# Performance work log

Hardware: AMD Instinct MI355X
Metric: run time of the kernel (lower is better)

## Reference

```python
import jax, jax.numpy as jnp
import numpy as np

N_NODES = 100000


def _sage_conv(x, src, dst, W_l, b_l, W_r, num_nodes):
    # PyG SAGEConv (aggr='mean'): out = lin_l(mean_j x_j) + lin_r(x)
    msg = x[src]                                                   # [E, d] gather
    s = jax.ops.segment_sum(msg, dst, num_segments=num_nodes)      # [N, d]
    cnt = jax.ops.segment_sum(jnp.ones((src.shape[0], 1), x.dtype), dst,
                              num_segments=num_nodes)              # [N, 1]
    agg = s / jnp.maximum(cnt, 1)                                  # mean, 0 if no neighbors
    return agg @ W_l.T + b_l + x @ W_r.T


def setup_inputs() -> dict:
    key = jax.random.key(0)
    ks = jax.random.split(key, 8)
    d = 64
    E = 1600000
    scale = 1.0 / np.sqrt(d)
    x = jax.random.normal(ks[0], (N_NODES, d), dtype=jnp.float32)
    edge_index = jax.random.randint(ks[1], (2, E), 0, N_NODES, dtype=jnp.int64)
    W1_l = jax.random.normal(ks[2], (d, d), dtype=jnp.float32) * scale
    b1_l = jnp.zeros((d,), dtype=jnp.float32)
    W1_r = jax.random.normal(ks[3], (d, d), dtype=jnp.float32) * scale
    W2_l = jax.random.normal(ks[4], (d, d), dtype=jnp.float32) * scale
    b2_l = jnp.zeros((d,), dtype=jnp.float32)
    W2_r = jax.random.normal(ks[5], (d, d), dtype=jnp.float32) * scale
    return {"x": x, "edge_index": edge_index, "W1_l": W1_l, "b1_l": b1_l,
            "W1_r": W1_r, "W2_l": W2_l, "b2_l": b2_l, "W2_r": W2_r}


def reference(x, edge_index, W1_l, b1_l, W1_r, W2_l, b2_l, W2_r):
    src, dst = edge_index[0], edge_index[1]
    h = jax.nn.relu(_sage_conv(x, src, dst, W1_l, b1_l, W1_r, N_NODES))
    h = jax.nn.relu(_sage_conv(h, src, dst, W2_l, b2_l, W2_r, N_NODES))
    return h
```

## Files before the change

kernel.cpp:

```cpp
#include <hip/hip_runtime.h>
#include <hip/hip_fp16.h>


#define NFEAT 64
#define NPB 128
#define NBUCK 782
#define MAXPB 2560
#define TILE 4096

typedef _Float16 h8 __attribute__((ext_vector_type(8)));
typedef _Float16 h4 __attribute__((ext_vector_type(4)));
typedef float f4 __attribute__((ext_vector_type(4)));
typedef float f2 __attribute__((ext_vector_type(2)));

__device__ inline h8 cvt8f(const float* p) {
  float4 lo = *(const float4*)p;
  float4 hi = *(const float4*)(p + 4);
  h8 f;
  f[0]=(_Float16)lo.x; f[1]=(_Float16)lo.y; f[2]=(_Float16)lo.z; f[3]=(_Float16)lo.w;
  f[4]=(_Float16)hi.x; f[5]=(_Float16)hi.y; f[6]=(_Float16)hi.z; f[7]=(_Float16)hi.w;
  return f;
}

__device__ inline void acc16(float* a, uint4 r) {
  f2 t;
  t = __builtin_amdgcn_cvt_pk_f32_fp8((int)r.x, false); a[0]+=t[0];  a[1]+=t[1];
  t = __builtin_amdgcn_cvt_pk_f32_fp8((int)r.x, true);  a[2]+=t[0];  a[3]+=t[1];
  t = __builtin_amdgcn_cvt_pk_f32_fp8((int)r.y, false); a[4]+=t[0];  a[5]+=t[1];
  t = __builtin_amdgcn_cvt_pk_f32_fp8((int)r.y, true);  a[6]+=t[0];  a[7]+=t[1];
  t = __builtin_amdgcn_cvt_pk_f32_fp8((int)r.z, false); a[8]+=t[0];  a[9]+=t[1];
  t = __builtin_amdgcn_cvt_pk_f32_fp8((int)r.z, true);  a[10]+=t[0]; a[11]+=t[1];
  t = __builtin_amdgcn_cvt_pk_f32_fp8((int)r.w, false); a[12]+=t[0]; a[13]+=t[1];
  t = __builtin_amdgcn_cvt_pk_f32_fp8((int)r.w, true);  a[14]+=t[0]; a[15]+=t[1];
}

__device__ inline void gather_team(float* a, const int* __restrict__ csr,
                                   const unsigned char* __restrict__ Z,
                                   int start, int deg, int q, int team) {
  int nfull = deg >> 2;
  for (int k = team; k < nfull; k += 2) {
    int j = start + k * 4;
    int n0 = csr[j + 0];
    int n1 = csr[j + 1];
    int n2 = csr[j + 2];
    int n3 = csr[j + 3];
    uint4 r0 = *(const uint4*)(Z + (size_t)n0 * NFEAT + q * 16);
    uint4 r1 = *(const uint4*)(Z + (size_t)n1 * NFEAT + q * 16);
    uint4 r2 = *(const uint4*)(Z + (size_t)n2 * NFEAT + q * 16);
    uint4 r3 = *(const uint4*)(Z + (size_t)n3 * NFEAT + q * 16);
    acc16(a, r0); acc16(a, r1); acc16(a, r2); acc16(a, r3);
  }
  int rem = deg & 3;
  if (rem && ((nfull & 1) == team)) {
    int j = start + nfull * 4;
    for (int i = 0; i < rem; ++i) {
      int nb = csr[j + i];
      uint4 r = *(const uint4*)(Z + (size_t)nb * NFEAT + q * 16);
      acc16(a, r);
    }
  }
}

__global__ __launch_bounds__(512) void build_gemm1_k(
    const int* __restrict__ src, const int* __restrict__ dst,
    int* __restrict__ gcur, int* __restrict__ pairs, int E, int sb,
    const float* __restrict__ X, const float* __restrict__ Wl,
    const float* __restrict__ Wr, const float* __restrict__ bias,
    unsigned char* __restrict__ Zf8, __half* __restrict__ Ph, int n) {
  int tid = threadIdx.x;
  if ((int)blockIdx.x < sb) {
    __shared__ int lcnt[NBUCK];
    __shared__ int loff[NBUCK];
    __shared__ int lcur[NBUCK];
    __shared__ int lbase[NBUCK];
    __shared__ int s_packed[TILE];
    __shared__ unsigned short s_b[TILE];

    int tileStart = blockIdx.x * TILE;
    int tileCnt = E - tileStart; if (tileCnt > TILE) tileCnt = TILE;

    for (int t = tid; t < NBUCK; t += 512) lcnt[t] = 0;
    __syncthreads();

    int ep[8], eb[8];
    int base = tileStart + tid * 8;
    int ne = 0;
    if (base + 7 < E) {
      int4 a0 = *(const int4*)(src + base);
      int4 a1 = *(const int4*)(src + base + 4);
      int4 b0 = *(const int4*)(dst + base);
      int4 b1 = *(const int4*)(dst + base + 4);
      int es[8] = {a0.x,a0.y,a0.z,a0.w,a1.x,a1.y,a1.z,a1.w};
      int ed[8] = {b0.x,b0.y,b0.z,b0.w,b1.x,b1.y,b1.z,b1.w};
#pragma unroll
      for (int j = 0; j < 8; ++j) {
        eb[j] = ed[j] >> 7;
        ep[j] = es[j] | ((ed[j] & 127) << 17);
      }
      ne = 8;
    } else {
      for (int j = 0; j < 8 && base + j < E; ++j) {
        int s = src[base + j], d = dst[base + j];
        eb[j] = d >> 7;
        ep[j] = s | ((d & 127) << 17);
        ++ne;
      }
    }
    for (int j = 0; j < ne; ++j) atomicAdd(&lcnt[eb[j]], 1);
    __syncthreads();

    if (tid < 64) {
      int carry = 0;
      for (int cb = 0; cb < NBUCK; cb += 64) {
        int i = cb + tid;
        int v = (i < NBUCK) ? lcnt[i] : 0;
        int x = v;
#pragma unroll
        for (int d = 1; d < 64; d <<= 1) {
          int y = __shfl_up(x, d);
          if (tid >= d) x += y;
        }
        if (i < NBUCK) { int e = x - v + carry; loff[i] = e; lcur[i] = e; }
        carry += __shfl(x, 63);
      }
    }
    __syncthreads();

    for (int t = tid; t < NBUCK; t += 512) {
      int v = lcnt[t];
      if (v) lbase[t] = atomicAdd(&gcur[t], v);
    }
    __syncthreads();

    for (int j = 0; j < ne; ++j) {
      int b = eb[j];
      int slot = atomicAdd(&lcur[b], 1);
      s_packed[slot] = ep[j];
      s_b[slot] = (unsigned short)b;
    }
    __syncthreads();

    for (int k = tid; k < tileCnt; k += 512) {
      int b = s_b[k];
      int g = lbase[b] + (k - loff[b]);
      if (g < MAXPB) pairs[(size_t)b * MAXPB + g] = s_packed[k];
    }
  } else {
    int wave = tid >> 6, lane = tid & 63;
    int m = lane & 15, quad = lane >> 4;
    int row0 = (((int)blockIdx.x - sb) * 8 + wave) * 16;
    if (row0 >= n) return;

    h8 wf[2][4][2];
#pragma unroll
    for (int mat = 0; mat < 2; ++mat) {
      const float* W = mat ? Wr : Wl;
#pragma unroll
      for (int t = 0; t < 4; ++t)
#pragma unroll
        for (int s = 0; s < 2; ++s)
          wf[mat][t][s] = cvt8f(W + (t * 16 + m) * 64 + s * 32 + quad * 8);
    }

    int rowm = row0 + m; if (rowm > n - 1) rowm = n - 1;
    const float* xp = X + (size_t)rowm * 64 + quad * 8;
    h8 af0 = cvt8f(xp);
    h8 af1 = cvt8f(xp + 32);

    f4 accz[4], accp[4];
#pragma unroll
    for (int t = 0; t < 4; ++t) {
      f4 z; z[0]=0.f; z[1]=0.f; z[2]=0.f; z[3]=0.f;
      float4 bl = *(const float4*)(bias + t * 16 + quad * 4);
      f4 p; p[0]=bl.x; p[1]=bl.y; p[2]=bl.z; p[3]=bl.w;
      z = __builtin_amdgcn_mfma_f32_16x16x32_f16(wf[0][t][0], af0, z, 0, 0, 0);
      z = __builtin_amdgcn_mfma_f32_16x16x32_f16(wf[0][t][1], af1, z, 0, 0, 0);
      p = __builtin_amdgcn_mfma_f32_16x16x32_f16(wf[1][t][0], af0, p, 0, 0, 0);
      p = __builtin_amdgcn_mfma_f32_16x16x32_f16(wf[1][t][1], af1, p, 0, 0, 0);
      accz[t] = z;
      accp[t] = p;
    }

    if (row0 + m < n) {
      size_t node = (size_t)(row0 + m);
#pragma unroll
      for (int t = 0; t < 4; ++t) {
        h4 pv;
#pragma unroll
        for (int r = 0; r < 4; ++r) pv[r] = (_Float16)accp[t][r];
        *(h4*)(Ph + node * NFEAT + t * 16 + quad * 4) = pv;
        int v = 0;
        v = __builtin_amdgcn_cvt_pk_fp8_f32(accz[t][0], accz[t][1], v, false);
        v = __builtin_amdgcn_cvt_pk_fp8_f32(accz[t][2], accz[t][3], v, true);
        *(int*)(Zf8 + node * NFEAT + t * 16 + quad * 4) = v;
      }
    }
  }
}

__global__ __launch_bounds__(512) void regroup_k(const int* __restrict__ gcur,
                                                 const int* __restrict__ pairs,
                                                 int* __restrict__ csr,
                                                 int* __restrict__ off,
                                                 int* __restrict__ cnt,
                                                 float* __restrict__ inv, int n) {
  __shared__ int lcnt[NPB];
  __shared__ int lofs[NPB];
  __shared__ int lcur[NPB];
  __shared__ int stage[MAXPB];

  int tid = threadIdx.x;
  int b = blockIdx.x;
  int nbase = b << 7;
  int nn = n - nbase; if (nn > NPB) nn = NPB;
  if (nn <= 0) return;

  int m = gcur[b]; if (m > MAXPB) m = MAXPB;
  const int* seg = pairs + (size_t)b * MAXPB;

  if (tid < NPB) lcnt[tid] = 0;
  __syncthreads();

  for (int e = tid; e < m; e += 512)
    atomicAdd(&lcnt[(seg[e] >> 17) & 127], 1);
  __syncthreads();

  if (tid < 64) {
    int carry = 0;
#pragma unroll
    for (int cb = 0; cb < NPB; cb += 64) {
      int i = cb + tid;
      int v = lcnt[i];
      int x = v;
#pragma unroll
      for (int d = 1; d < 64; d <<= 1) {
        int y = __shfl_up(x, d);
        if (tid >= d) x += y;
      }
      int e = x - v + carry;
      lofs[i] = e; lcur[i] = e;
      carry += __shfl(x, 63);
    }
  }
  __syncthreads();

  for (int e = tid; e < m; e += 512) {
    int p = seg[e];
    int slot = atomicAdd(&lcur[(p >> 17) & 127], 1);
    stage[slot] = p & 0x1FFFF;
  }
  __syncthreads();

  for (int k = tid; k < m; k += 512) csr[(size_t)b * MAXPB + k] = stage[k];
  for (int t = tid; t < nn; t += 512) {
    int c = lcnt[t];
    cnt[nbase + t] = c;
    off[nbase + t] = b * MAXPB + lofs[t];
    inv[nbase + t] = 1.0f / (float)(c > 1 ? c : 1);
  }
}

__global__ __launch_bounds__(256) void aggemm_k(
    const int* __restrict__ off, const int* __restrict__ cnt,
    const float* __restrict__ inv, const int* __restrict__ csr,
    const unsigned char* __restrict__ Z, const __half* __restrict__ Pin,
    const float* __restrict__ Wl, const float* __restrict__ Wr,
    const float* __restrict__ bias,
    unsigned char* __restrict__ Zout, __half* __restrict__ Pout, int n) {
  __shared__ _Float16 Hs[32][72];
  int tid = threadIdx.x;
  int nbase = blockIdx.x * 32;
  int nl   = tid >> 3;
  int t8   = tid & 7;
  int q    = t8 & 3;
  int team = t8 >> 2;
  int node = nbase + nl;

  float a[16];
#pragma unroll
  for (int i = 0; i < 16; ++i) a[i] = 0.f;

  if (node < n) {
    gather_team(a, csr, Z, off[node], cnt[node], q, team);
  }
#pragma unroll
  for (int i = 0; i < 16; ++i) a[i] += __shfl_xor(a[i], 4);

  if (node < n) {
    float iv = inv[node];
    if (team == 0) {
      h8 p0 = *(const h8*)(Pin + (size_t)node * NFEAT + q * 16);
      h8 h0;
#pragma unroll
      for (int i = 0; i < 8; ++i)
        h0[i] = (_Float16)fmaxf(fmaf(a[i], iv, (float)p0[i]), 0.f);
      *(h8*)&Hs[nl][q * 16] = h0;
    } else {
      h8 p1 = *(const h8*)(Pin + (size_t)node * NFEAT + q * 16 + 8);
      h8 h1;
#pragma unroll
      for (int i = 0; i < 8; ++i)
        h1[i] = (_Float16)fmaxf(fmaf(a[8 + i], iv, (float)p1[i]), 0.f);
      *(h8*)&Hs[nl][q * 16 + 8] = h1;
    }
  } else if (team == 0) {
    h8 zz;
#pragma unroll
    for (int i = 0; i < 8; ++i) zz[i] = (_Float16)0.f;
    *(h8*)&Hs[nl][q * 16] = zz;
    *(h8*)&Hs[nl][q * 16 + 8] = zz;
  }
  __syncthreads();

  int wave = tid >> 6, lane = tid & 63;
  if (wave >= 2) return;
  int m = lane & 15, quad = lane >> 4;
  int row0 = wave * 16;

  h8 wf[2][4][2];
#pragma unroll
  for (int mat = 0; mat < 2; ++mat) {
    const float* W = mat ? Wr : Wl;
#pragma unroll
    for (int t = 0; t < 4; ++t)
#pragma unroll
      for (int s = 0; s < 2; ++s)
        wf[mat][t][s] = cvt8f(W + (t * 16 + m) * 64 + s * 32 + quad * 8);
  }

  h8 af0 = *(const h8*)&Hs[row0 + m][quad * 8];
  h8 af1 = *(const h8*)&Hs[row0 + m][32 + quad * 8];

  f4 accz[4], accp[4];
#pragma unroll
  for (int t = 0; t < 4; ++t) {
    f4 z; z[0]=0.f; z[1]=0.f; z[2]=0.f; z[3]=0.f;
    float4 bl = *(const float4*)(bias + t * 16 + quad * 4);
    f4 p; p[0]=bl.x; p[1]=bl.y; p[2]=bl.z; p[3]=bl.w;
    z = __builtin_amdgcn_mfma_f32_16x16x32_f16(wf[0][t][0], af0, z, 0, 0, 0);
    z = __builtin_amdgcn_mfma_f32_16x16x32_f16(wf[0][t][1], af1, z, 0, 0, 0);
    p = __builtin_amdgcn_mfma_f32_16x16x32_f16(wf[1][t][0], af0, p, 0, 0, 0);
    p = __builtin_amdgcn_mfma_f32_16x16x32_f16(wf[1][t][1], af1, p, 0, 0, 0);
    accz[t] = z;
    accp[t] = p;
  }

  int gnode = nbase + row0 + m;
  if (gnode < n) {
    size_t nodeix = (size_t)gnode;
#pragma unroll
    for (int t = 0; t < 4; ++t) {
      h4 pv;
#pragma unroll
      for (int r = 0; r < 4; ++r) pv[r] = (_Float16)accp[t][r];
      *(h4*)(Pout + nodeix * NFEAT + t * 16 + quad * 4) = pv;
      int v = 0;
      v = __builtin_amdgcn_cvt_pk_fp8_f32(accz[t][0], accz[t][1], v, false);
      v = __builtin_amdgcn_cvt_pk_fp8_f32(accz[t][2], accz[t][3], v, true);
      *(int*)(Zout + nodeix * NFEAT + t * 16 + quad * 4) = v;
    }
  }
}

__global__ __launch_bounds__(256) void agg2_k(const int* __restrict__ off,
                                              const int* __restrict__ cnt,
                                              const float* __restrict__ inv,
                                              const int* __restrict__ csr,
                                              const unsigned char* __restrict__ Z,
                                              const __half* __restrict__ Pin,
                                              float* __restrict__ out, int n) {
  int t = blockIdx.x * 256 + threadIdx.x;
  int node = t >> 3;
  if (node >= n) return;
  int t8   = t & 7;
  int q    = t8 & 3;
  int team = t8 >> 2;

  float a[16];
#pragma unroll
  for (int i = 0; i < 16; ++i) a[i] = 0.f;

  gather_team(a, csr, Z, off[node], cnt[node], q, team);
#pragma unroll
  for (int i = 0; i < 16; ++i) a[i] += __shfl_xor(a[i], 4);

  float iv = inv[node];
  float* op = out + (size_t)node * NFEAT + q * 16;
  if (team == 0) {
    h8 p0 = *(const h8*)(Pin + (size_t)node * NFEAT + q * 16);
    float4 r0, r1;
    r0.x = fmaxf(fmaf(a[0], iv, (float)p0[0]), 0.f);
    r0.y = fmaxf(fmaf(a[1], iv, (float)p0[1]), 0.f);
    r0.z = fmaxf(fmaf(a[2], iv, (float)p0[2]), 0.f);
    r0.w = fmaxf(fmaf(a[3], iv, (float)p0[3]), 0.f);
    r1.x = fmaxf(fmaf(a[4], iv, (float)p0[4]), 0.f);
    r1.y = fmaxf(fmaf(a[5], iv, (float)p0[5]), 0.f);
    r1.z = fmaxf(fmaf(a[6], iv, (float)p0[6]), 0.f);
    r1.w = fmaxf(fmaf(a[7], iv, (float)p0[7]), 0.f);
    *(float4*)(op + 0) = r0;
    *(float4*)(op + 4) = r1;
  } else {
    h8 p1 = *(const h8*)(Pin + (size_t)node * NFEAT + q * 16 + 8);
    float4 r2, r3;
    r2.x = fmaxf(fmaf(a[8],  iv, (float)p1[0]), 0.f);
    r2.y = fmaxf(fmaf(a[9],  iv, (float)p1[1]), 0.f);
    r2.z = fmaxf(fmaf(a[10], iv, (float)p1[2]), 0.f);
    r2.w = fmaxf(fmaf(a[11], iv, (float)p1[3]), 0.f);
    r3.x = fmaxf(fmaf(a[12], iv, (float)p1[4]), 0.f);
    r3.y = fmaxf(fmaf(a[13], iv, (float)p1[5]), 0.f);
    r3.z = fmaxf(fmaf(a[14], iv, (float)p1[6]), 0.f);
    r3.w = fmaxf(fmaf(a[15], iv, (float)p1[7]), 0.f);
    *(float4*)(op + 8)  = r2;
    *(float4*)(op + 12) = r3;
  }
}

extern "C" void kernel_launch(void* const* d_in, const int* in_sizes, int n_in,
                              void* d_out, int out_size, void* d_ws, size_t ws_size,
                              hipStream_t stream) {
  const float* x   = (const float*)d_in[0];
  const int*   ei  = (const int*)d_in[1];
  const float* W1l = (const float*)d_in[2];
  const float* b1  = (const float*)d_in[3];
  const float* W1r = (const float*)d_in[4];
  const float* W2l = (const float*)d_in[5];
  const float* b2  = (const float*)d_in[6];
  const float* W2r = (const float*)d_in[7];
  float* out = (float*)d_out;

  int N = in_sizes[0] / NFEAT;
  int E = in_sizes[1] / 2;
  const int* srcp = ei;
  const int* dstp = ei + E;

  char* w = (char*)d_ws;
  int*           pairs = (int*)w;           w += (size_t)NBUCK * MAXPB * 4;
  int*           csr   = (int*)w;           w += (size_t)NBUCK * MAXPB * 4;
  unsigned char* Z1    = (unsigned char*)w; w += (size_t)N * NFEAT;
  __half*        P1    = (__half*)w;        w += (size_t)N * NFEAT * 2;
  unsigned char* Z2    = (unsigned char*)w; w += (size_t)N * NFEAT;
  __half*        P2    = (__half*)w;        w += (size_t)N * NFEAT * 2;
  int*           off   = (int*)w;           w += (size_t)N * 4;
  int*           cnt   = (int*)w;           w += (size_t)N * 4;
  float*         inv   = (float*)w;         w += (size_t)N * 4;
  int*           gcur  = (int*)w;           w += NBUCK * 4;
  if ((size_t)(w - (char*)d_ws) > ws_size) return;

  hipMemsetAsync(gcur, 0, NBUCK * 4, stream);

  int sb  = (E + TILE - 1) / TILE;
  int gb1 = (N + 127) / 128;

  build_gemm1_k<<<sb + gb1, 512, 0, stream>>>(srcp, dstp, gcur, pairs, E, sb,
                                              x, W1l, W1r, b1, Z1, P1, N);
  regroup_k<<<NBUCK, 512, 0, stream>>>(gcur, pairs, csr, off, cnt, inv, N);
  aggemm_k<<<(N + 31) / 32, 256, 0, stream>>>(off, cnt, inv, csr, Z1, P1,
                                              W2l, W2r, b2, Z2, P2, N);
  agg2_k<<<(N * 8 + 255) / 256, 256, 0, stream>>>(off, cnt, inv, csr, Z2, P2,
                                                  out, N);
}
```

Measured before the change: 232.9 us.

## Fuse CSR regroup with layer-2 aggregation GEMM and split layer-2 features into planes

Merges the regroup kernel and the first aggregation+GEMM kernel into one 1024-thread block per 128-node bucket, reading neighbor indices straight from shared memory instead of writing and re-reading the CSR from global memory. This also removes a kernel launch. Layer-2 fp8 features are now stored as two 32-byte half planes, and the final aggregation kernel runs one block set per plane with four teams per node, so each plane's gather footprint is smaller and more cache-friendly. The cost is larger blocks with lower occupancy and bucket-granularity parallelism (782 blocks) for the gather phase.

```diff
diff --git a/kernel.cpp b/kernel.cpp
--- a/kernel.cpp
+++ b/kernel.cpp
@@ -32,33 +32,6 @@
   t = __builtin_amdgcn_cvt_pk_f32_fp8((int)r.z, true);  a[10]+=t[0]; a[11]+=t[1];
   t = __builtin_amdgcn_cvt_pk_f32_fp8((int)r.w, false); a[12]+=t[0]; a[13]+=t[1];
   t = __builtin_amdgcn_cvt_pk_f32_fp8((int)r.w, true);  a[14]+=t[0]; a[15]+=t[1];
-}
-
-__device__ inline void gather_team(float* a, const int* __restrict__ csr,
-                                   const unsigned char* __restrict__ Z,
-                                   int start, int deg, int q, int team) {
-  int nfull = deg >> 2;
-  for (int k = team; k < nfull; k += 2) {
-    int j = start + k * 4;
-    int n0 = csr[j + 0];
-    int n1 = csr[j + 1];
-    int n2 = csr[j + 2];
-    int n3 = csr[j + 3];
-    uint4 r0 = *(const uint4*)(Z + (size_t)n0 * NFEAT + q * 16);
-    uint4 r1 = *(const uint4*)(Z + (size_t)n1 * NFEAT + q * 16);
-    uint4 r2 = *(const uint4*)(Z + (size_t)n2 * NFEAT + q * 16);
-    uint4 r3 = *(const uint4*)(Z + (size_t)n3 * NFEAT + q * 16);
-    acc16(a, r0); acc16(a, r1); acc16(a, r2); acc16(a, r3);
-  }
-  int rem = deg & 3;
-  if (rem && ((nfull & 1) == team)) {
-    int j = start + nfull * 4;
-    for (int i = 0; i < rem; ++i) {
-      int nb = csr[j + i];
-      uint4 r = *(const uint4*)(Z + (size_t)nb * NFEAT + q * 16);
-      acc16(a, r);
-    }
-  }
 }
 
 __global__ __launch_bounds__(512) void build_gemm1_k(
@@ -198,16 +171,20 @@
   }
 }
 
-__global__ __launch_bounds__(512) void regroup_k(const int* __restrict__ gcur,
-                                                 const int* __restrict__ pairs,
-                                                 int* __restrict__ csr,
-                                                 int* __restrict__ off,
-                                                 int* __restrict__ cnt,
-                                                 float* __restrict__ inv, int n) {
+__global__ __launch_bounds__(1024) void raggemm_k(
+    const int* __restrict__ gcur, const int* __restrict__ pairs,
+    int* __restrict__ csr, int* __restrict__ off,
+    int* __restrict__ cnt, float* __restrict__ inv,
+    const unsigned char* __restrict__ Z, const __half* __restrict__ Pin,
+    const float* __restrict__ Wl, const float* __restrict__ Wr,
+    const float* __restrict__ bias,
+    unsigned char* __restrict__ Zlo, unsigned char* __restrict__ Zhi,
+    __half* __restrict__ Pout, int n) {
   __shared__ int lcnt[NPB];
   __shared__ int lofs[NPB];
   __shared__ int lcur[NPB];
   __shared__ int stage[MAXPB];
+  __shared__ _Float16 Hs[NPB][72];
 
   int tid = threadIdx.x;
   int b = blockIdx.x;
@@ -221,7 +198,7 @@
   if (tid < NPB) lcnt[tid] = 0;
   __syncthreads();
 
-  for (int e = tid; e < m; e += 512)
+  for (int e = tid; e < m; e += 1024)
     atomicAdd(&lcnt[(seg[e] >> 17) & 127], 1);
   __syncthreads();
 
@@ -244,32 +221,21 @@
   }
   __syncthreads();
 
-  for (int e = tid; e < m; e += 512) {
+  for (int e = tid; e < m; e += 1024) {
     int p = seg[e];
     int slot = atomicAdd(&lcur[(p >> 17) & 127], 1);
     stage[slot] = p & 0x1FFFF;
   }
   __syncthreads();
 
-  for (int k = tid; k < m; k += 512) csr[(size_t)b * MAXPB + k] = stage[k];
-  for (int t = tid; t < nn; t += 512) {
+  for (int k = tid; k < m; k += 1024) csr[(size_t)b * MAXPB + k] = stage[k];
+  for (int t = tid; t < nn; t += 1024) {
     int c = lcnt[t];
     cnt[nbase + t] = c;
     off[nbase + t] = b * MAXPB + lofs[t];
     inv[nbase + t] = 1.0f / (float)(c > 1 ? c : 1);
   }
-}
-
-__global__ __launch_bounds__(256) void aggemm_k(
-    const int* __restrict__ off, const int* __restrict__ cnt,
-    const float* __restrict__ inv, const int* __restrict__ csr,
-    const unsigned char* __restrict__ Z, const __half* __restrict__ Pin,
-    const float* __restrict__ Wl, const float* __restrict__ Wr,
-    const float* __restrict__ bias,
-    unsigned char* __restrict__ Zout, __half* __restrict__ Pout, int n) {
-  __shared__ _Float16 Hs[32][72];
-  int tid = threadIdx.x;
-  int nbase = blockIdx.x * 32;
+
   int nl   = tid >> 3;
   int t8   = tid & 7;
   int q    = t8 & 3;
@@ -280,14 +246,37 @@
 #pragma unroll
   for (int i = 0; i < 16; ++i) a[i] = 0.f;
 
+  int deg = 0, start = 0;
+  if (node < n) { deg = lcnt[nl]; start = lofs[nl]; }
+  {
+    int nfull = deg >> 2;
+    for (int k = team; k < nfull; k += 2) {
+      int j = start + k * 4;
+      int n0 = stage[j + 0];
+      int n1 = stage[j + 1];
+      int n2 = stage[j + 2];
+      int n3 = stage[j + 3];
+      uint4 r0 = *(const uint4*)(Z + (size_t)n0 * NFEAT + q * 16);
+      uint4 r1 = *(const uint4*)(Z + (size_t)n1 * NFEAT + q * 16);
+      uint4 r2 = *(const uint4*)(Z + (size_t)n2 * NFEAT + q * 16);
+      uint4 r3 = *(const uint4*)(Z + (size_t)n3 * NFEAT + q * 16);
+      acc16(a, r0); acc16(a, r1); acc16(a, r2); acc16(a, r3);
+    }
+    int rem = deg & 3;
+    if (rem && ((nfull & 1) == team)) {
+      int j = start + nfull * 4;
+      for (int i = 0; i < rem; ++i) {
+        int nb = stage[j + i];
+        uint4 r = *(const uint4*)(Z + (size_t)nb * NFEAT + q * 16);
+        acc16(a, r);
+      }
+    }
+  }
+#pragma unroll
+  for (int i = 0; i < 16; ++i) a[i] += __shfl_xor(a[i], 4);
+
   if (node < n) {
-    gather_team(a, csr, Z, off[node], cnt[node], q, team);
-  }
-#pragma unroll
-  for (int i = 0; i < 16; ++i) a[i] += __shfl_xor(a[i], 4);
-
-  if (node < n) {
-    float iv = inv[node];
+    float iv = 1.0f / (float)(deg > 1 ? deg : 1);
     if (team == 0) {
       h8 p0 = *(const h8*)(Pin + (size_t)node * NFEAT + q * 16);
       h8 h0;
@@ -313,8 +302,8 @@
   __syncthreads();
 
   int wave = tid >> 6, lane = tid & 63;
-  if (wave >= 2) return;
-  int m = lane & 15, quad = lane >> 4;
+  if (wave >= 8) return;
+  int mm = lane & 15, quad = lane >> 4;
   int row0 = wave * 16;
 
   h8 wf[2][4][2];
@@ -325,11 +314,11 @@
     for (int t = 0; t < 4; ++t)
 #pragma unroll
       for (int s = 0; s < 2; ++s)
-        wf[mat][t][s] = cvt8f(W + (t * 16 + m) * 64 + s * 32 + quad * 8);
-  }
-
-  h8 af0 = *(const h8*)&Hs[row0 + m][quad * 8];
-  h8 af1 = *(const h8*)&Hs[row0 + m][32 + quad * 8];
+        wf[mat][t][s] = cvt8f(W + (t * 16 + mm) * 64 + s * 32 + quad * 8);
+  }
+
+  h8 af0 = *(const h8*)&Hs[row0 + mm][quad * 8];
+  h8 af1 = *(const h8*)&Hs[row0 + mm][32 + quad * 8];
 
   f4 accz[4], accp[4];
 #pragma unroll
@@ -345,7 +334,7 @@
     accp[t] = p;
   }
 
-  int gnode = nbase + row0 + m;
+  int gnode = nbase + row0 + mm;
   if (gnode < n) {
     size_t nodeix = (size_t)gnode;
 #pragma unroll
@@ -357,7 +346,8 @@
       int v = 0;
       v = __builtin_amdgcn_cvt_pk_fp8_f32(accz[t][0], accz[t][1], v, false);
       v = __builtin_amdgcn_cvt_pk_fp8_f32(accz[t][2], accz[t][3], v, true);
-      *(int*)(Zout + nodeix * NFEAT + t * 16 + quad * 4) = v;
+      unsigned char* zp = (t < 2) ? Zlo : Zhi;
+      *(int*)(zp + nodeix * 32 + (t & 1) * 16 + quad * 4) = v;
     }
   }
 }
@@ -366,42 +356,70 @@
                                               const int* __restrict__ cnt,
                                               const float* __restrict__ inv,
                                               const int* __restrict__ csr,
-                                              const unsigned char* __restrict__ Z,
+                                              const unsigned char* __restrict__ Zlo,
+                                              const unsigned char* __restrict__ Zhi,
                                               const __half* __restrict__ Pin,
-                                              float* __restrict__ out, int n) {
-  int t = blockIdx.x * 256 + threadIdx.x;
-  int node = t >> 3;
+                                              float* __restrict__ out,
+                                              int n, int nchunk) {
+  int bi = blockIdx.x;
+  int plane = (bi >= nchunk) ? 1 : 0;
+  int chunk = plane ? bi - nchunk : bi;
+  int tid = threadIdx.x;
+  int nl = tid >> 3;
+  int node = chunk * 32 + nl;
   if (node >= n) return;
-  int t8   = t & 7;
-  int q    = t8 & 3;
-  int team = t8 >> 2;
+  int t8   = tid & 7;
+  int half = t8 & 1;
+  int team = t8 >> 1;
+  const unsigned char* Zp = plane ? Zhi : Zlo;
 
   float a[16];
 #pragma unroll
   for (int i = 0; i < 16; ++i) a[i] = 0.f;
 
-  gather_team(a, csr, Z, off[node], cnt[node], q, team);
+  int start = off[node];
+  int deg = cnt[node];
+  int nfull = deg >> 2;
+  for (int k = team; k < nfull; k += 4) {
+    int j = start + k * 4;
+    int n0 = csr[j + 0];
+    int n1 = csr[j + 1];
+    int n2 = csr[j + 2];
+    int n3 = csr[j + 3];
+    uint4 r0 = *(const uint4*)(Zp + (size_t)n0 * 32 + half * 16);
+    uint4 r1 = *(const uint4*)(Zp + (size_t)n1 * 32 + half * 16);
+    uint4 r2 = *(const uint4*)(Zp + (size_t)n2 * 32 + half * 16);
+    uint4 r3 = *(const uint4*)(Zp + (size_t)n3 * 32 + half * 16);
+    acc16(a, r0); acc16(a, r1); acc16(a, r2); acc16(a, r3);
+  }
+  int rem = deg & 3;
+  if (rem && ((nfull & 3) == team)) {
+    int j = start + nfull * 4;
+    for (int i = 0; i < rem; ++i) {
+      int nb = csr[j + i];
+      uint4 r = *(const uint4*)(Zp + (size_t)nb * 32 + half * 16);
+      acc16(a, r);
+    }
+  }
+#pragma unroll
+  for (int i = 0; i < 16; ++i) a[i] += __shfl_xor(a[i], 2);
 #pragma unroll
   for (int i = 0; i < 16; ++i) a[i] += __shfl_xor(a[i], 4);
 
-  float iv = inv[node];
-  float* op = out + (size_t)node * NFEAT + q * 16;
   if (team == 0) {
-    h8 p0 = *(const h8*)(Pin + (size_t)node * NFEAT + q * 16);
-    float4 r0, r1;
-    r0.x = fmaxf(fmaf(a[0], iv, (float)p0[0]), 0.f);
-    r0.y = fmaxf(fmaf(a[1], iv, (float)p0[1]), 0.f);
-    r0.z = fmaxf(fmaf(a[2], iv, (float)p0[2]), 0.f);
-    r0.w = fmaxf(fmaf(a[3], iv, (float)p0[3]), 0.f);
-    r1.x = fmaxf(fmaf(a[4], iv, (float)p0[4]), 0.f);
-    r1.y = fmaxf(fmaf(a[5], iv, (float)p0[5]), 0.f);
-    r1.z = fmaxf(fmaf(a[6], iv, (float)p0[6]), 0.f);
-    r1.w = fmaxf(fmaf(a[7], iv, (float)p0[7]), 0.f);
-    *(float4*)(op + 0) = r0;
-    *(float4*)(op + 4) = r1;
-  } else {
-    h8 p1 = *(const h8*)(Pin + (size_t)node * NFEAT + q * 16 + 8);
-    float4 r2, r3;
+    float iv = inv[node];
+    int fbase = plane * 32 + half * 16;
+    h8 p0 = *(const h8*)(Pin + (size_t)node * NFEAT + fbase);
+    h8 p1 = *(const h8*)(Pin + (size_t)node * NFEAT + fbase + 8);
+    float4 r0, r1, r2, r3;
+    r0.x = fmaxf(fmaf(a[0],  iv, (float)p0[0]), 0.f);
+    r0.y = fmaxf(fmaf(a[1],  iv, (float)p0[1]), 0.f);
+    r0.z = fmaxf(fmaf(a[2],  iv, (float)p0[2]), 0.f);
+    r0.w = fmaxf(fmaf(a[3],  iv, (float)p0[3]), 0.f);
+    r1.x = fmaxf(fmaf(a[4],  iv, (float)p0[4]), 0.f);
+    r1.y = fmaxf(fmaf(a[5],  iv, (float)p0[5]), 0.f);
+    r1.z = fmaxf(fmaf(a[6],  iv, (float)p0[6]), 0.f);
+    r1.w = fmaxf(fmaf(a[7],  iv, (float)p0[7]), 0.f);
     r2.x = fmaxf(fmaf(a[8],  iv, (float)p1[0]), 0.f);
     r2.y = fmaxf(fmaf(a[9],  iv, (float)p1[1]), 0.f);
     r2.z = fmaxf(fmaf(a[10], iv, (float)p1[2]), 0.f);
@@ -410,6 +428,9 @@
     r3.y = fmaxf(fmaf(a[13], iv, (float)p1[5]), 0.f);
     r3.z = fmaxf(fmaf(a[14], iv, (float)p1[6]), 0.f);
     r3.w = fmaxf(fmaf(a[15], iv, (float)p1[7]), 0.f);
+    float* op = out + (size_t)node * NFEAT + fbase;
+    *(float4*)(op + 0)  = r0;
+    *(float4*)(op + 4)  = r1;
     *(float4*)(op + 8)  = r2;
     *(float4*)(op + 12) = r3;
   }
@@ -446,16 +467,20 @@
   int*           gcur  = (int*)w;           w += NBUCK * 4;
   if ((size_t)(w - (char*)d_ws) > ws_size) return;
 
+  unsigned char* Z2lo = Z2;
+  unsigned char* Z2hi = Z2 + (size_t)N * 32;
+
   hipMemsetAsync(gcur, 0, NBUCK * 4, stream);
 
   int sb  = (E + TILE - 1) / TILE;
   int gb1 = (N + 127) / 128;
+  int nchunk = (N + 31) / 32;
 
   build_gemm1_k<<<sb + gb1, 512, 0, stream>>>(srcp, dstp, gcur, pairs, E, sb,
                                               x, W1l, W1r, b1, Z1, P1, N);
-  regroup_k<<<NBUCK, 512, 0, stream>>>(gcur, pairs, csr, off, cnt, inv, N);
-  aggemm_k<<<(N + 31) / 32, 256, 0, stream>>>(off, cnt, inv, csr, Z1, P1,
-                                              W2l, W2r, b2, Z2, P2, N);
-  agg2_k<<<(N * 8 + 255) / 256, 256, 0, stream>>>(off, cnt, inv, csr, Z2, P2,
-                                                  out, N);
-}
+  raggemm_k<<<NBUCK, 1024, 0, stream>>>(gcur, pairs, csr, off, cnt, inv,
+                                        Z1, P1, W2l, W2r, b2,
+                                        Z2lo, Z2hi, P2, N);
+  agg2_k<<<2 * nchunk, 256, 0, stream>>>(off, cnt, inv, csr, Z2lo, Z2hi, P2,
+                                         out, N, nchunk);
+}
```

Result: slower. 251.3 us (+7.9%).
